# Performance work log

Measured on AMD Instinct MI355X. Metric: run time of the kernel, lower is better.

Reference implementation:

```python
import jax, jax.numpy as jnp
import numpy as np

B, P, M, N, H = 2, 2048, 1024, 16, 64
NEG = 1e10


def setup_inputs() -> dict:
    key = jax.random.key(0)
    ks = jax.random.split(key, 8)
    std = 0.02
    return {
        "x": jax.random.normal(ks[0], (B, P, M), jnp.float32),
        "kernel_query": std * jax.random.normal(ks[1], (N, M, H), jnp.float32),
        "bias_query": jnp.zeros((N, H), jnp.float32),
        "kernel_key": std * jax.random.normal(ks[2], (N, M, H), jnp.float32),
        "bias_key": jnp.zeros((N, H), jnp.float32),
        "kernel_value": std * jax.random.normal(ks[3], (N, M, H), jnp.float32),
        "bias_value": jnp.zeros((N, H), jnp.float32),
        "kernel_out": std * jax.random.normal(ks[4], (N, H, M), jnp.float32),
        "bias_out": jnp.zeros((M,), jnp.float32),
    }


def reference(x, kernel_query, bias_query, kernel_key, bias_key,
              kernel_value, bias_value, kernel_out, bias_out):
    # per-head projections: [b,p,m] x [n,m,h] -> [b,p,n,h]
    q = jnp.einsum('bpm,nmh->bpnh', x, kernel_query) + bias_query
    k = jnp.einsum('bpm,nmh->bpnh', x, kernel_key) + bias_key
    v = jnp.einsum('bpm,nmh->bpnh', x, kernel_value) + bias_value

    # explicit score matrix [b,n,pq,pk]
    scores = jnp.einsum('bqnh,bknh->bnqk', q, k) / jnp.sqrt(jnp.float32(H))
    # faithful reproduction of original (inverted) mask: keep strictly-upper
    # triangle, subtract 1e10 elsewhere
    p = scores.shape[-1]
    mask = jnp.triu(jnp.ones((p, p), scores.dtype), k=1)  # [pq,pk]
    masked = scores * mask - NEG * (1.0 - mask)
    attn = jax.nn.softmax(masked, axis=-1)

    z = jnp.einsum('bknh,bnqk->bqnh', v, attn)
    return jnp.einsum('bqnh,nhm->bqm', z, kernel_out) + bias_out
```

## Files before the change

### kernel.cpp

```cpp
#include <hip/hip_runtime.h>

typedef __attribute__((ext_vector_type(8))) __bf16 bf16x8;
typedef __attribute__((ext_vector_type(4))) float  f32x4;
typedef unsigned short u16;
typedef unsigned int   u32;

__device__ __forceinline__ u16 f2b(float f) {
  u32 u = __builtin_bit_cast(u32, f);
  u32 r = (u + 0x7FFFu + ((u >> 16) & 1u)) >> 16;
  return (u16)r;
}

typedef __attribute__((address_space(3))) void lds_void;
typedef const __attribute__((address_space(1))) void gbl_void;

__device__ __forceinline__ void gload_lds16(const u16* g, u16* l) {
  __builtin_amdgcn_global_load_lds((gbl_void*)g, (lds_void*)l, 16, 0, 0);
}

#define QSCALE 0.18033688011112042f
#define MFIX   4.328085122666891f

__global__ __launch_bounds__(256) void prep_all(const float* __restrict__ x,
                                                const float* __restrict__ wq,
                                                const float* __restrict__ wk,
                                                const float* __restrict__ wv,
                                                const float* __restrict__ wo,
                                                u16* __restrict__ xb,
                                                u16* __restrict__ wbt,
                                                u16* __restrict__ wot) {
  int bid = blockIdx.x;
  int tid = threadIdx.x;
  if (bid < 4096) {
    int i = bid * 256 + tid;
    float4 v = ((const float4*)x)[i];
    ushort4 o;
    o.x = f2b(v.x); o.y = f2b(v.y); o.z = f2b(v.z); o.w = f2b(v.w);
    ((ushort4*)xb)[i] = o;
    return;
  }
  __shared__ float t[64][65];
  int sub = bid - 4096;
  const float* src; u16* dst; int sstride, dstride, r0, c0;
  if (sub < 768) {
    int proj = sub >> 8, rem = sub & 255;
    int ym = rem >> 4, xt = rem & 15;
    src = ((proj == 0) ? wq : (proj == 1) ? wk : wv) + (size_t)ym * 65536;
    dst = wbt + ((size_t)proj << 20) + (size_t)ym * 65536;
    sstride = 64; dstride = 1024; r0 = xt * 64; c0 = 0;
  } else {
    int s2 = sub - 768;
    src = wo; dst = wot;
    sstride = 1024; dstride = 1024;
    r0 = (s2 & 15) * 64; c0 = (s2 >> 4) * 64;
  }
  int rr = tid >> 2, q = tid & 3;
#pragma unroll
  for (int i = 0; i < 4; ++i) {
    float4 v = *(const float4*)&src[(size_t)(r0 + rr) * sstride + c0 + q * 16 + i * 4];
    t[rr][q * 16 + i * 4 + 0] = v.x;
    t[rr][q * 16 + i * 4 + 1] = v.y;
    t[rr][q * 16 + i * 4 + 2] = v.z;
    t[rr][q * 16 + i * 4 + 3] = v.w;
  }
  __syncthreads();
  int cc = rr;
#pragma unroll
  for (int i = 0; i < 4; ++i) {
    ushort4 o;
    o.x = f2b(t[q * 16 + i * 4 + 0][cc]);
    o.y = f2b(t[q * 16 + i * 4 + 1][cc]);
    o.z = f2b(t[q * 16 + i * 4 + 2][cc]);
    o.w = f2b(t[q * 16 + i * 4 + 3][cc]);
    *(ushort4*)&dst[(size_t)(c0 + cc) * dstride + r0 + q * 16 + i * 4] = o;
  }
}

template <int KDIM>
__device__ __forceinline__ void gemm_main(const u16* __restrict__ A,
                                          const u16* __restrict__ Bm,
                                          int R0, int C0,
                                          u16* As, u16* Bs, f32x4 (&acc)[4][4]) {
  int tid = threadIdx.x;
  int w = tid >> 6, l = tid & 63;
  int lr = l & 15, lg = l >> 4;
  int wr = w >> 1, wc = w & 1;
  for (int k0 = 0; k0 < KDIM; k0 += 32) {
#pragma unroll
    for (int i = 0; i < 2; ++i) {
      int t = w * 2 + i;
      gload_lds16(A  + (size_t)(R0 + t * 16 + (l >> 2)) * KDIM + k0 + (l & 3) * 8, &As[t * 512]);
      gload_lds16(Bm + (size_t)(C0 + t * 16 + (l >> 2)) * KDIM + k0 + (l & 3) * 8, &Bs[t * 512]);
    }
    __syncthreads();
    bf16x8 af[4], bfr[4];
#pragma unroll
    for (int mi = 0; mi < 4; ++mi)
      af[mi] = *(const bf16x8*)&As[(wr * 64 + mi * 16 + lr) * 32 + lg * 8];
#pragma unroll
    for (int ni = 0; ni < 4; ++ni)
      bfr[ni] = *(const bf16x8*)&Bs[(wc * 64 + ni * 16 + lr) * 32 + lg * 8];
#pragma unroll
    for (int mi = 0; mi < 4; ++mi)
#pragma unroll
      for (int ni = 0; ni < 4; ++ni)
        acc[mi][ni] = __builtin_amdgcn_mfma_f32_16x16x32_bf16(af[mi], bfr[ni], acc[mi][ni], 0, 0, 0);
    __syncthreads();
  }
}

__global__ __launch_bounds__(256) void gemm_qkv(const u16* __restrict__ xb,
                                                const u16* __restrict__ wbt,
                                                const float* __restrict__ bq,
                                                const float* __restrict__ bk,
                                                const float* __restrict__ bv,
                                                u16* __restrict__ qb,
                                                u16* __restrict__ kbf,
                                                u16* __restrict__ vtb) {
  __shared__ __align__(16) u16 SH[2][4096];
  f32x4 acc[4][4];
#pragma unroll
  for (int mi = 0; mi < 4; ++mi)
#pragma unroll
    for (int ni = 0; ni < 4; ++ni) acc[mi][ni] = (f32x4){0.f, 0.f, 0.f, 0.f};

  int bid = blockIdx.x;
  int rt = bid & 31, ct = bid >> 5;
  int R0 = rt * 128, C0 = ct * 128;
  gemm_main<1024>(xb, wbt, R0, C0, SH[0], SH[1], acc);

  int tid = threadIdx.x;
  int w = tid >> 6, l = tid & 63;
  int lr = l & 15, lg = l >> 4;
  int wr = w >> 1, wc = w & 1;

  int proj = C0 >> 10;
  int colbase = C0 + wc * 64;
  int n = (colbase & 1023) >> 6;
  int rowbase = R0 + wr * 64;
  int b = rowbase >> 11, p0 = rowbase & 2047;
  int bn = b * 16 + n;

  if (proj < 2) {
    const float* bias = (proj == 0) ? bq : bk;
    float scl = (proj == 0) ? QSCALE : 1.0f;
    u16* dst = ((proj == 0) ? qb : kbf) + ((size_t)bn * 2048 + p0) * 64;
#pragma unroll
    for (int ni = 0; ni < 4; ++ni) {
      float badd = bias[n * 64 + ni * 16 + lr];
#pragma unroll
      for (int mi = 0; mi < 4; ++mi)
#pragma unroll
        for (int r = 0; r < 4; ++r)
          dst[(size_t)(mi * 16 + lg * 4 + r) * 64 + ni * 16 + lr] =
              f2b((acc[mi][ni][r] + badd) * scl);
    }
  } else {
    int pblk = p0 >> 6;
    u16* dst = vtb + ((size_t)bn * 32 + pblk) * 4096;
    u16* Tw = &SH[0][0] + w * 2048;
#pragma unroll
    for (int hh = 0; hh < 2; ++hh) {
#pragma unroll
      for (int nn = 0; nn < 2; ++nn) {
        int ni = hh * 2 + nn;
        float badd = bv[n * 64 + ni * 16 + lr];
        int hloc = nn * 16 + lr;
#pragma unroll
        for (int mi = 0; mi < 4; ++mi)
#pragma unroll
          for (int r = 0; r < 4; ++r) {
            int ploc = mi * 16 + lg * 4 + r;
            Tw[hloc * 64 + ((((ploc >> 3) ^ (hloc & 7)) << 3) | (ploc & 7))] =
                f2b(acc[mi][ni][r] + badd);
          }
      }
      asm volatile("s_waitcnt lgkmcnt(0)" ::: "memory");
      __builtin_amdgcn_sched_barrier(0);
#pragma unroll
      for (int pp = 0; pp < 4; ++pp) {
        int hloc = pp * 8 + (l >> 3);
        int ccn = l & 7;
        bf16x8 vv = *(const bf16x8*)&Tw[hloc * 64 + ((ccn ^ (hloc & 7)) << 3)];
        *(bf16x8*)&dst[(size_t)(hh * 32 + hloc) * 64 + ccn * 8] = vv;
      }
    }
  }
}

__global__ __launch_bounds__(256) void mean_v(const u16* __restrict__ vtb,
                                              u16* __restrict__ zb) {
  __shared__ float red[4][64];
  int bn = blockIdx.x;
  int w = threadIdx.x >> 6, h = threadIdx.x & 63;
  const u16* base = vtb + (size_t)bn * 131072 + (size_t)h * 64;
  float acc = 0.f;
  for (int pb = w; pb < 32; pb += 4) {
    const u16* r = base + (size_t)pb * 4096;
#pragma unroll
    for (int c = 0; c < 8; ++c) {
      bf16x8 v = *(const bf16x8*)(r + c * 8);
#pragma unroll
      for (int j = 0; j < 8; ++j) acc += (float)v[j];
    }
  }
  red[w][h] = acc;
  __syncthreads();
  if (w == 0) {
    float s = (red[0][h] + red[1][h] + red[2][h] + red[3][h]) * (1.0f / 2048.0f);
    int b = bn >> 4, n = bn & 15;
    zb[((size_t)(b * 2048 + 2047) * 16 + n) * 64 + h] = f2b(s);
  }
}

#define ATTN_STEP(BUFC, MASKED)                                                \
  {                                                                            \
    if (t + 1 < trips) {                                                       \
      gload_lds16(sk,       &Ks[BUFC ^ 1][w * 1024]);                          \
      gload_lds16(sk + 512, &Ks[BUFC ^ 1][w * 1024 + 512]);                    \
      gload_lds16(sv,       &Vs[BUFC ^ 1][w * 1024]);                          \
      gload_lds16(sv + 512, &Vs[BUFC ^ 1][w * 1024 + 512]);                    \
      sk += 4096; sv += 4096;                                                  \
      asm volatile("s_waitcnt vmcnt(4)" ::: "memory");                         \
    } else {                                                                   \
      asm volatile("s_waitcnt vmcnt(0)" ::: "memory");                         \
    }                                                                          \
    __builtin_amdgcn_s_barrier();                                              \
    asm volatile("" ::: "memory");                                             \
    f32x4 sacc[4];                                                             \
    __builtin_amdgcn_s_setprio(1);                                             \
    _Pragma("unroll") for (int nb = 0; nb < 4; ++nb) {                         \
      int row = nb * 16 + lr, sw = row & 7;                                    \
      bf16x8 kf0 = *(const bf16x8*)&Ks[BUFC][row * 64 + ((lg ^ sw) << 3)];     \
      bf16x8 kf1 = *(const bf16x8*)&Ks[BUFC][row * 64 + (((lg + 4) ^ sw) << 3)]; \
      f32x4 s = (f32x4){0.f, 0.f, 0.f, 0.f};                                   \
      s = __builtin_amdgcn_mfma_f32_16x16x32_bf16(qf0, kf0, s, 0, 0, 0);       \
      s = __builtin_amdgcn_mfma_f32_16x16x32_bf16(qf1, kf1, s, 0, 0, 0);       \
      sacc[nb] = s;                                                            \
    }                                                                          \
    __builtin_amdgcn_s_setprio(0);                                             \
    u16 pbv[4][4];                                                             \
    if (MASKED) {                                                              \
      _Pragma("unroll") for (int nb = 0; nb < 4; ++nb) {                       \
        int key = nb * 16 + lr;                                                \
        _Pragma("unroll") for (int r = 0; r < 4; ++r) {                        \
          int qrow = w * 16 + lg * 4 + r;                                      \
          float xv = (key > qrow) ? sacc[nb][r] : -1.0e10f;                    \
          float pe = __builtin_amdgcn_exp2f(xv - MFIX);                        \
          rsum[r] += pe;                                                       \
          pbv[nb][r] = __builtin_bit_cast(u16, (__bf16)pe);                    \
        }                                                                      \
      }                                                                        \
    } else {                                                                   \
      _Pragma("unroll") for (int nb = 0; nb < 4; ++nb)                         \
        _Pragma("unroll") for (int r = 0; r < 4; ++r) {                        \
          float pe = __builtin_amdgcn_exp2f(sacc[nb][r] - MFIX);               \
          rsum[r] += pe;                                                       \
          pbv[nb][r] = __builtin_bit_cast(u16, (__bf16)pe);                    \
        }                                                                      \
    }                                                                          \
    _Pragma("unroll") for (int nb = 0; nb < 4; ++nb)                           \
      _Pragma("unroll") for (int r = 0; r < 4; ++r) {                          \
        int prow = lg * 4 + r;                                                 \
        Plds[w][prow * 64 + ((((nb * 2) + (lr >> 3)) ^ (prow & 7)) << 3) + (lr & 7)] = pbv[nb][r]; \
      }                                                                        \
    asm volatile("s_waitcnt lgkmcnt(0)" ::: "memory");                         \
    __builtin_amdgcn_sched_barrier(0);                                         \
    bf16x8 pf0 = *(const bf16x8*)&Plds[w][lr * 64 + ((lg ^ (lr & 7)) << 3)];   \
    bf16x8 pf1 = *(const bf16x8*)&Plds[w][lr * 64 + (((4 + lg) ^ (lr & 7)) << 3)]; \
    __builtin_amdgcn_s_setprio(1);                                             \
    _Pragma("unroll") for (int hb = 0; hb < 4; ++hb) {                         \
      int row = hb * 16 + lr, sw = row & 7;                                    \
      bf16x8 vf0 = *(const bf16x8*)&Vs[BUFC][row * 64 + ((lg ^ sw) << 3)];     \
      bf16x8 vf1 = *(const bf16x8*)&Vs[BUFC][row * 64 + (((lg + 4) ^ sw) << 3)]; \
      oacc[hb] = __builtin_amdgcn_mfma_f32_16x16x32_bf16(pf0, vf0, oacc[hb], 0, 0, 0); \
      oacc[hb] = __builtin_amdgcn_mfma_f32_16x16x32_bf16(pf1, vf1, oacc[hb], 0, 0, 0); \
    }                                                                          \
    __builtin_amdgcn_s_setprio(0);                                             \
    asm volatile("" ::: "memory");                                             \
    __builtin_amdgcn_s_barrier();                                              \
    ++t;                                                                       \
  }

__global__ __launch_bounds__(256, 4) void attn_kern(const u16* __restrict__ qb,
                                                    const u16* __restrict__ kbf,
                                                    const u16* __restrict__ vtb,
                                                    u16* __restrict__ zb) {
  __shared__ __align__(16) u16 Ks[2][4096];
  __shared__ __align__(16) u16 Vs[2][4096];
  __shared__ __align__(16) u16 Plds[4][1024];

  int bid = blockIdx.x;
  int bn = bid & 31, c = bid >> 5;
  int trips = 32 - c;
  int tid = threadIdx.x;
  int w = tid >> 6, l = tid & 63;
  int lr = l & 15, lg = l >> 4;

  const u16* Q  = qb  + (size_t)bn * 131072;
  const u16* Kp = kbf + (size_t)bn * 131072;
  const u16* Vt = vtb + (size_t)bn * 131072;

  int row0 = w * 16 + (l >> 3), col8 = l & 7;
  int soff = row0 * 64 + ((col8 ^ (row0 & 7)) << 3);

  int q0w = c * 64 + w * 16;
  bf16x8 qf0 = *(const bf16x8*)&Q[(size_t)(q0w + lr) * 64 + lg * 8];
  bf16x8 qf1 = *(const bf16x8*)&Q[(size_t)(q0w + lr) * 64 + 32 + lg * 8];

  float rsum[4];
  f32x4 oacc[4];
#pragma unroll
  for (int r = 0; r < 4; ++r) rsum[r] = 0.0f;
#pragma unroll
  for (int hb = 0; hb < 4; ++hb) oacc[hb] = (f32x4){0.f, 0.f, 0.f, 0.f};

  const u16* sk = Kp + (size_t)c * 4096 + soff;
  const u16* sv = Vt + (size_t)c * 4096 + soff;
  gload_lds16(sk,       &Ks[0][w * 1024]);
  gload_lds16(sk + 512, &Ks[0][w * 1024 + 512]);
  gload_lds16(sv,       &Vs[0][w * 1024]);
  gload_lds16(sv + 512, &Vs[0][w * 1024 + 512]);
  sk += 4096; sv += 4096;

  int t = 0;
  ATTN_STEP(0, true)
  while (t + 1 < trips) {
    ATTN_STEP(1, false)
    ATTN_STEP(0, false)
  }
  if (t < trips) ATTN_STEP(1, false)

#pragma unroll
  for (int r = 0; r < 4; ++r) {
    float v = rsum[r];
    v += __shfl_xor(v, 1);
    v += __shfl_xor(v, 2);
    v += __shfl_xor(v, 4);
    v += __shfl_xor(v, 8);
    rsum[r] = 1.0f / v;
  }
  int b = bn >> 4, n = bn & 15;
#pragma unroll
  for (int hb = 0; hb < 4; ++hb) {
    int h = hb * 16 + lr;
#pragma unroll
    for (int r = 0; r < 4; ++r) {
      int qrow = q0w + lg * 4 + r;
      zb[((size_t)(b * 2048 + qrow) * 16 + n) * 64 + h] = f2b(oacc[hb][r] * rsum[r]);
    }
  }
}

__global__ __launch_bounds__(256) void gemm_out(const u16* __restrict__ zb,
                                                const u16* __restrict__ wot,
                                                const float* __restrict__ bo,
                                                float* __restrict__ out) {
  __shared__ __align__(16) u16 As[128 * 32];
  __shared__ __align__(16) u16 Bs[128 * 32];
  f32x4 acc[4][4];
#pragma unroll
  for (int mi = 0; mi < 4; ++mi)
#pragma unroll
    for (int ni = 0; ni < 4; ++ni) acc[mi][ni] = (f32x4){0.f, 0.f, 0.f, 0.f};

  int bid = blockIdx.x;
  int rt = bid & 31, ct = bid >> 5;
  int R0 = rt * 128, C0 = ct * 128;
  gemm_main<1024>(zb, wot, R0, C0, As, Bs, acc);

  int tid = threadIdx.x;
  int w = tid >> 6, l = tid & 63;
  int lr = l & 15, lg = l >> 4;
  int wr = w >> 1, wc = w & 1;
#pragma unroll
  for (int ni = 0; ni < 4; ++ni) {
    int col = C0 + wc * 64 + ni * 16 + lr;
    float badd = bo[col];
#pragma unroll
    for (int mi = 0; mi < 4; ++mi) {
#pragma unroll
      for (int r = 0; r < 4; ++r) {
        int row = R0 + wr * 64 + mi * 16 + lg * 4 + r;
        out[(size_t)row * 1024 + col] = acc[mi][ni][r] + badd;
      }
    }
  }
}

extern "C" void kernel_launch(void* const* d_in, const int* in_sizes, int n_in,
                              void* d_out, int out_size, void* d_ws, size_t ws_size,
                              hipStream_t stream) {
  const float* x  = (const float*)d_in[0];
  const float* wq = (const float*)d_in[1];
  const float* bq = (const float*)d_in[2];
  const float* wk = (const float*)d_in[3];
  const float* bk = (const float*)d_in[4];
  const float* wv = (const float*)d_in[5];
  const float* bv = (const float*)d_in[6];
  const float* wo = (const float*)d_in[7];
  const float* bo = (const float*)d_in[8];
  float* out = (float*)d_out;

  char* ws = (char*)d_ws;
  u16* xb  = (u16*)(ws + ((size_t)0 << 20));
  u16* wbt = (u16*)(ws + ((size_t)8 << 20));
  u16* wot = (u16*)(ws + ((size_t)14 << 20));
  u16* qb  = (u16*)(ws + ((size_t)16 << 20));
  u16* kbf = (u16*)(ws + ((size_t)24 << 20));
  u16* vtb = (u16*)(ws + ((size_t)32 << 20));
  u16* zb  = (u16*)(ws + ((size_t)40 << 20));

  prep_all<<<dim3(5120), dim3(256), 0, stream>>>(x, wq, wk, wv, wo, xb, wbt, wot);
  gemm_qkv<<<dim3(32 * 24), dim3(256), 0, stream>>>(xb, wbt, bq, bk, bv, qb, kbf, vtb);
  attn_kern<<<dim3(1024), dim3(256), 0, stream>>>(qb, kbf, vtb, zb);
  mean_v<<<dim3(32), dim3(256), 0, stream>>>(vtb, zb);
  gemm_out<<<dim3(32 * 8), dim3(256), 0, stream>>>(zb, wot, bo, out);
}
```

Before: 128.3 us.

## Remap GEMM block order, narrow output GEMM tiles, simplify QKV epilogue stores

The QKV GEMM now reorders block indices so consecutive blocks are spread across eight groups. Its V-transpose epilogue, which staged through LDS, is replaced by direct scalar scattered stores for all three projections. The output GEMM switches to 128x64 tiles with an inline K loop, launching twice as many blocks (512) to fill more compute units, and also gets a remapped block order. The scattered 2-byte stores for V (stride 64 elements) and the loss of vectorised writes could raise store cost in exchange.

New measurement: 130.6 us. About the same (+1.8%).

```diff
diff --git a/kernel.cpp b/kernel.cpp
--- a/kernel.cpp
+++ b/kernel.cpp
@@ -117,72 +117,43 @@
                                                 u16* __restrict__ qb,
                                                 u16* __restrict__ kbf,
                                                 u16* __restrict__ vtb) {
-  __shared__ __align__(16) u16 SH[2][4096];
+  __shared__ __align__(16) u16 As[128 * 32];
+  __shared__ __align__(16) u16 Bs[128 * 32];
   f32x4 acc[4][4];
 #pragma unroll
   for (int mi = 0; mi < 4; ++mi)
 #pragma unroll
     for (int ni = 0; ni < 4; ++ni) acc[mi][ni] = (f32x4){0.f, 0.f, 0.f, 0.f};
 
-  int bid = blockIdx.x;
+  int bid = (blockIdx.x & 7) * 96 + (blockIdx.x >> 3);
   int rt = bid & 31, ct = bid >> 5;
   int R0 = rt * 128, C0 = ct * 128;
-  gemm_main<1024>(xb, wbt, R0, C0, SH[0], SH[1], acc);
+  gemm_main<1024>(xb, wbt, R0, C0, As, Bs, acc);
 
   int tid = threadIdx.x;
   int w = tid >> 6, l = tid & 63;
   int lr = l & 15, lg = l >> 4;
   int wr = w >> 1, wc = w & 1;
-
-  int proj = C0 >> 10;
-  int colbase = C0 + wc * 64;
-  int n = (colbase & 1023) >> 6;
-  int rowbase = R0 + wr * 64;
-  int b = rowbase >> 11, p0 = rowbase & 2047;
-  int bn = b * 16 + n;
-
-  if (proj < 2) {
-    const float* bias = (proj == 0) ? bq : bk;
+#pragma unroll
+  for (int ni = 0; ni < 4; ++ni) {
+    int col = C0 + wc * 64 + ni * 16 + lr;
+    int proj = col >> 10;
+    int within = col & 1023;
+    int n = within >> 6, h = within & 63;
+    const float* bias = (proj == 0) ? bq : (proj == 1 ? bk : bv);
+    float badd = bias[within];
     float scl = (proj == 0) ? QSCALE : 1.0f;
-    u16* dst = ((proj == 0) ? qb : kbf) + ((size_t)bn * 2048 + p0) * 64;
-#pragma unroll
-    for (int ni = 0; ni < 4; ++ni) {
-      float badd = bias[n * 64 + ni * 16 + lr];
-#pragma unroll
-      for (int mi = 0; mi < 4; ++mi)
-#pragma unroll
-        for (int r = 0; r < 4; ++r)
-          dst[(size_t)(mi * 16 + lg * 4 + r) * 64 + ni * 16 + lr] =
-              f2b((acc[mi][ni][r] + badd) * scl);
-    }
-  } else {
-    int pblk = p0 >> 6;
-    u16* dst = vtb + ((size_t)bn * 32 + pblk) * 4096;
-    u16* Tw = &SH[0][0] + w * 2048;
-#pragma unroll
-    for (int hh = 0; hh < 2; ++hh) {
-#pragma unroll
-      for (int nn = 0; nn < 2; ++nn) {
-        int ni = hh * 2 + nn;
-        float badd = bv[n * 64 + ni * 16 + lr];
-        int hloc = nn * 16 + lr;
-#pragma unroll
-        for (int mi = 0; mi < 4; ++mi)
-#pragma unroll
-          for (int r = 0; r < 4; ++r) {
-            int ploc = mi * 16 + lg * 4 + r;
-            Tw[hloc * 64 + ((((ploc >> 3) ^ (hloc & 7)) << 3) | (ploc & 7))] =
-                f2b(acc[mi][ni][r] + badd);
-          }
-      }
-      asm volatile("s_waitcnt lgkmcnt(0)" ::: "memory");
-      __builtin_amdgcn_sched_barrier(0);
-#pragma unroll
-      for (int pp = 0; pp < 4; ++pp) {
-        int hloc = pp * 8 + (l >> 3);
-        int ccn = l & 7;
-        bf16x8 vv = *(const bf16x8*)&Tw[hloc * 64 + ((ccn ^ (hloc & 7)) << 3)];
-        *(bf16x8*)&dst[(size_t)(hh * 32 + hloc) * 64 + ccn * 8] = vv;
+#pragma unroll
+    for (int mi = 0; mi < 4; ++mi) {
+#pragma unroll
+      for (int r = 0; r < 4; ++r) {
+        int row = R0 + wr * 64 + mi * 16 + lg * 4 + r;
+        int b = row >> 11, p = row & 2047;
+        int bn = b * 16 + n;
+        u16 u = f2b((acc[mi][ni][r] + badd) * scl);
+        if (proj == 0)      qb [((size_t)bn * 2048 + p) * 64 + h] = u;
+        else if (proj == 1) kbf[((size_t)bn * 2048 + p) * 64 + h] = u;
+        else                vtb[(((size_t)bn * 32 + (p >> 6)) * 64 + h) * 64 + (p & 63)] = u;
       }
     }
   }
@@ -357,25 +328,48 @@
                                                 const float* __restrict__ bo,
                                                 float* __restrict__ out) {
   __shared__ __align__(16) u16 As[128 * 32];
-  __shared__ __align__(16) u16 Bs[128 * 32];
-  f32x4 acc[4][4];
+  __shared__ __align__(16) u16 Bs[64 * 32];
+  f32x4 acc[4][2];
 #pragma unroll
   for (int mi = 0; mi < 4; ++mi)
 #pragma unroll
-    for (int ni = 0; ni < 4; ++ni) acc[mi][ni] = (f32x4){0.f, 0.f, 0.f, 0.f};
-
-  int bid = blockIdx.x;
-  int rt = bid & 31, ct = bid >> 5;
-  int R0 = rt * 128, C0 = ct * 128;
-  gemm_main<1024>(zb, wot, R0, C0, As, Bs, acc);
+    for (int ni = 0; ni < 2; ++ni) acc[mi][ni] = (f32x4){0.f, 0.f, 0.f, 0.f};
+
+  int bid = (blockIdx.x & 7) * 64 + (blockIdx.x >> 3);
+  int rt = bid >> 4, ct = bid & 15;
+  int R0 = rt * 128, C0 = ct * 64;
 
   int tid = threadIdx.x;
   int w = tid >> 6, l = tid & 63;
   int lr = l & 15, lg = l >> 4;
   int wr = w >> 1, wc = w & 1;
-#pragma unroll
-  for (int ni = 0; ni < 4; ++ni) {
-    int col = C0 + wc * 64 + ni * 16 + lr;
+
+  for (int k0 = 0; k0 < 1024; k0 += 32) {
+#pragma unroll
+    for (int i = 0; i < 2; ++i) {
+      int t = w * 2 + i;
+      gload_lds16(zb + (size_t)(R0 + t * 16 + (l >> 2)) * 1024 + k0 + (l & 3) * 8, &As[t * 512]);
+    }
+    gload_lds16(wot + (size_t)(C0 + w * 16 + (l >> 2)) * 1024 + k0 + (l & 3) * 8, &Bs[w * 512]);
+    __syncthreads();
+    bf16x8 af[4], bfr[2];
+#pragma unroll
+    for (int mi = 0; mi < 4; ++mi)
+      af[mi] = *(const bf16x8*)&As[(wr * 64 + mi * 16 + lr) * 32 + lg * 8];
+#pragma unroll
+    for (int ni = 0; ni < 2; ++ni)
+      bfr[ni] = *(const bf16x8*)&Bs[(wc * 32 + ni * 16 + lr) * 32 + lg * 8];
+#pragma unroll
+    for (int mi = 0; mi < 4; ++mi)
+#pragma unroll
+      for (int ni = 0; ni < 2; ++ni)
+        acc[mi][ni] = __builtin_amdgcn_mfma_f32_16x16x32_bf16(af[mi], bfr[ni], acc[mi][ni], 0, 0, 0);
+    __syncthreads();
+  }
+
+#pragma unroll
+  for (int ni = 0; ni < 2; ++ni) {
+    int col = C0 + wc * 32 + ni * 16 + lr;
     float badd = bo[col];
 #pragma unroll
     for (int mi = 0; mi < 4; ++mi) {
@@ -415,5 +409,5 @@
   gemm_qkv<<<dim3(32 * 24), dim3(256), 0, stream>>>(xb, wbt, bq, bk, bv, qb, kbf, vtb);
   attn_kern<<<dim3(1024), dim3(256), 0, stream>>>(qb, kbf, vtb, zb);
   mean_v<<<dim3(32), dim3(256), 0, stream>>>(vtb, zb);
-  gemm_out<<<dim3(32 * 8), dim3(256), 0, stream>>>(zb, wot, bo, out);
-}
+  gemm_out<<<dim3(32 * 16), dim3(256), 0, stream>>>(zb, wot, bo, out);
+}
```
